# Kernel optimization log

Measured on AMD Instinct MI355X. Metric: run time of the kernel, lower is better.

Reference implementation:

```python
import jax, jax.numpy as jnp
import numpy as np

N_EMBD = 1024
N_HEAD = 16
B, T = 2, 2048

def setup_inputs() -> dict:
    key = jax.random.key(0)
    ks = jax.random.split(key, 5)
    s = 1.0 / np.sqrt(N_EMBD)
    return {
        'x': jax.random.normal(ks[0], (B, T, N_EMBD), jnp.float32),
        'W_attn': jax.random.normal(ks[1], (N_EMBD, 3 * N_EMBD), jnp.float32) * s,
        'b_attn': jax.random.normal(ks[2], (3 * N_EMBD,), jnp.float32) * 0.02,
        'W_proj': jax.random.normal(ks[3], (N_EMBD, N_EMBD), jnp.float32) * s,
        'b_proj': jax.random.normal(ks[4], (N_EMBD,), jnp.float32) * 0.02,
    }

def reference(x, W_attn, b_attn, W_proj, b_proj):
    Bx, Tx, C = x.shape
    H = N_HEAD
    D = C // H  # head dim
    qkv = x @ W_attn + b_attn                      # [B,T,3C]
    q, k, v = jnp.split(qkv, 3, axis=-1)
    # [B,T,C] -> [B,H,T,D]
    q = q.reshape(Bx, Tx, H, D).transpose(0, 2, 1, 3)
    k = k.reshape(Bx, Tx, H, D).transpose(0, 2, 1, 3)
    v = v.reshape(Bx, Tx, H, D).transpose(0, 2, 1, 3)
    scale = 1.0 / jnp.sqrt(jnp.asarray(D, x.dtype))
    scores = jnp.einsum('bhqd,bhkd->bhqk', q, k) * scale   # [B,H,T,T]
    causal = jnp.tril(jnp.ones((Tx, Tx), bool))
    scores = jnp.where(causal, scores, jnp.asarray(-jnp.inf, scores.dtype))
    attn = jax.nn.softmax(scores, axis=-1)
    y = jnp.einsum('bhqk,bhkd->bhqd', attn, v)              # [B,H,T,D]
    y = y.transpose(0, 2, 1, 3).reshape(Bx, Tx, C)
    return y @ W_proj + b_proj
```

## Files before the change

### kernel.cpp

```cpp
#include <hip/hip_runtime.h>
#include <stdint.h>

typedef float f32x4 __attribute__((ext_vector_type(4)));
typedef __bf16 bf16x8 __attribute__((ext_vector_type(8)));
typedef unsigned short ushort8 __attribute__((ext_vector_type(8)));
typedef unsigned short u16;

#define DEVINL static __device__ __forceinline__

#define EXP2(x) exp2f(x)

#define VMCNT(N)                                        \
  {                                                     \
    asm volatile("s_waitcnt vmcnt(" #N ")" ::: "memory"); \
    __builtin_amdgcn_sched_barrier(0);                  \
  }

DEVINL void barrier_raw() {
  __builtin_amdgcn_sched_barrier(0);
  __builtin_amdgcn_s_barrier();
  __builtin_amdgcn_sched_barrier(0);
}

DEVINL u16 f2bf(float f) {
  __bf16 h = (__bf16)f;
  return __builtin_bit_cast(u16, h);
}

DEVINL void gload16(const void* g, void* l) {
  __builtin_amdgcn_global_load_lds((__attribute__((address_space(1))) void*)g,
                                   (__attribute__((address_space(3))) void*)l, 16, 0, 0);
}

DEVINL f32x4 mfma16(bf16x8 a, bf16x8 b, f32x4 c) {
  return __builtin_amdgcn_mfma_f32_16x16x32_bf16(a, b, c, 0, 0, 0);
}

__global__ __launch_bounds__(256) void k_cast_bf16(const float* __restrict__ in,
                                                   u16* __restrict__ out) {
  const int i = blockIdx.x * 256 + threadIdx.x;
  const float4* p = (const float4*)in + (size_t)i * 2;
  float4 a = p[0], b = p[1];
  ushort8 o;
  o[0] = f2bf(a.x); o[1] = f2bf(a.y); o[2] = f2bf(a.z); o[3] = f2bf(a.w);
  o[4] = f2bf(b.x); o[5] = f2bf(b.y); o[6] = f2bf(b.z); o[7] = f2bf(b.w);
  *((ushort8*)out + i) = o;
}

__global__ __launch_bounds__(256) void k_tcast(const float* __restrict__ in,
                                               u16* __restrict__ out, int R, int C) {
  __shared__ float tile[32][33];
  const int tx = threadIdx.x & 31, ty = threadIdx.x >> 5;
  const int c0 = blockIdx.x * 32, r0 = blockIdx.y * 32;
#pragma unroll
  for (int k = 0; k < 4; ++k)
    tile[ty + k * 8][tx] = in[(size_t)(r0 + ty + k * 8) * C + (c0 + tx)];
  __syncthreads();
#pragma unroll
  for (int k = 0; k < 4; ++k)
    out[(size_t)(c0 + ty + k * 8) * R + (r0 + tx)] = f2bf(tile[tx][ty + k * 8]);
}

DEVINL void stage128x64(const u16* __restrict__ g, int ld, u16* lds, int t) {
#pragma unroll
  for (int i = 0; i < 4; ++i) {
    int ci = i * 256 + t;
    int row = ci >> 3, gr = ci & 7;
    int gs = gr ^ (row & 7);
    gload16(g + (size_t)row * ld + gs * 8, lds + ci * 8);
  }
}

DEVINL void gemm_core(const u16* __restrict__ A, const u16* __restrict__ B, int Kdim,
                      u16* As, u16* Bs, int t, f32x4 acc[4][4]) {
  const int l = t & 63, lr = l & 15, lg = l >> 4;
  const int wr = t >> 7, wc = (t >> 6) & 1;
  const int nk = Kdim >> 6;
  stage128x64(A, Kdim, As, t);
  stage128x64(B, Kdim, Bs, t);
  for (int kt = 0; kt < nk; ++kt) {
    if (kt + 1 < nk) {
      const int nx = ((kt + 1) & 1) * 8192;
      stage128x64(A + (kt + 1) * 64, Kdim, As + nx, t);
      stage128x64(B + (kt + 1) * 64, Kdim, Bs + nx, t);
      VMCNT(8);
    } else {
      VMCNT(0);
    }
    barrier_raw();
    const u16* Asc = As + (kt & 1) * 8192;
    const u16* Bsc = Bs + (kt & 1) * 8192;
#pragma unroll
    for (int ks = 0; ks < 2; ++ks) {
      bf16x8 af[4], bf[4];
#pragma unroll
      for (int mi = 0; mi < 4; ++mi) {
        int r = wr * 64 + mi * 16 + lr;
        int g = (ks * 4 + lg) ^ (r & 7);
        af[mi] = *(const bf16x8*)(Asc + r * 64 + g * 8);
      }
#pragma unroll
      for (int ni = 0; ni < 4; ++ni) {
        int r = wc * 64 + ni * 16 + lr;
        int g = (ks * 4 + lg) ^ (r & 7);
        bf[ni] = *(const bf16x8*)(Bsc + r * 64 + g * 8);
      }
#pragma unroll
      for (int mi = 0; mi < 4; ++mi)
#pragma unroll
        for (int ni = 0; ni < 4; ++ni)
          acc[mi][ni] = mfma16(af[mi], bf[ni], acc[mi][ni]);
    }
    barrier_raw();
  }
}

__global__ __launch_bounds__(256) void k_gemm_qkv(const u16* __restrict__ xb,
                                                  const u16* __restrict__ WaT,
                                                  const float* __restrict__ b_attn,
                                                  u16* __restrict__ Qo,
                                                  u16* __restrict__ Ko,
                                                  u16* __restrict__ Vto) {
  __shared__ u16 As[2 * 128 * 64], Bs[2 * 128 * 64];
  const int t = threadIdx.x;
  const int m0 = blockIdx.y * 128, n0 = blockIdx.x * 128;
  f32x4 acc[4][4] = {};
  gemm_core(xb + (size_t)m0 * 1024, WaT + (size_t)n0 * 1024, 1024, As, Bs, t, acc);
  const int l = t & 63, lr = l & 15, lg = l >> 4;
  const int wr = t >> 7, wc = (t >> 6) & 1;
#pragma unroll
  for (int ni = 0; ni < 4; ++ni) {
    const int gcol = n0 + wc * 64 + ni * 16 + lr;
    const int part = gcol >> 10;
    const int h = (gcol & 1023) >> 6, d = gcol & 63;
    const float bias = b_attn[gcol];
    if (part == 2) {
#pragma unroll
      for (int mi = 0; mi < 4; ++mi) {
        const int tt0 = m0 + wr * 64 + mi * 16 + lg * 4;
        const int bb = tt0 >> 11, tt = tt0 & 2047;
        ushort4 pk;
        pk.x = f2bf(acc[mi][ni][0] + bias);
        pk.y = f2bf(acc[mi][ni][1] + bias);
        pk.z = f2bf(acc[mi][ni][2] + bias);
        pk.w = f2bf(acc[mi][ni][3] + bias);
        *(ushort4*)(Vto + (size_t)(bb * 16 + h) * 131072 + (size_t)d * 2048 + tt) = pk;
      }
    } else {
      const float osc = (part == 0) ? 0.18033688f : 1.0f;
      u16* dst = (part == 0) ? Qo : Ko;
#pragma unroll
      for (int mi = 0; mi < 4; ++mi)
#pragma unroll
        for (int r = 0; r < 4; ++r) {
          const int grow = m0 + wr * 64 + mi * 16 + lg * 4 + r;
          const int bb = grow >> 11, tt = grow & 2047;
          dst[(size_t)((bb * 16 + h) * 2048 + tt) * 64 + d] =
              f2bf((acc[mi][ni][r] + bias) * osc);
        }
    }
  }
}

__global__ __launch_bounds__(256) void k_gemm_proj(const u16* __restrict__ Yb,
                                                   const u16* __restrict__ WpT,
                                                   const float* __restrict__ b_proj,
                                                   float* __restrict__ out) {
  __shared__ u16 As[2 * 128 * 64], Bs[2 * 128 * 64];
  const int t = threadIdx.x;
  const int m0 = blockIdx.y * 128, n0 = blockIdx.x * 128;
  f32x4 acc[4][4] = {};
  gemm_core(Yb + (size_t)m0 * 1024, WpT + (size_t)n0 * 1024, 1024, As, Bs, t, acc);
  const int l = t & 63, lr = l & 15, lg = l >> 4;
  const int wr = t >> 7, wc = (t >> 6) & 1;
#pragma unroll
  for (int ni = 0; ni < 4; ++ni) {
    const int gcol = n0 + wc * 64 + ni * 16 + lr;
    const float bias = b_proj[gcol];
#pragma unroll
    for (int mi = 0; mi < 4; ++mi)
#pragma unroll
      for (int r = 0; r < 4; ++r) {
        const int grow = m0 + wr * 64 + mi * 16 + lg * 4 + r;
        out[(size_t)grow * 1024 + gcol] = acc[mi][ni][r] + bias;
      }
  }
}

__global__ __launch_bounds__(512, 4) void k_flash(const u16* __restrict__ Q,
                                                  const u16* __restrict__ K,
                                                  const u16* __restrict__ Vt,
                                                  u16* __restrict__ Y) {
  __shared__ u16 Ks[2][64 * 64];
  __shared__ u16 Vs[2][64 * 64];
  __shared__ u16 Pl[8][16 * 40];
  __shared__ float Ms[4][64][18];
  const int t = threadIdx.x, l = t & 63, w = t >> 6, lr = l & 15, lg = l >> 4;
  const int wq = w & 3, wk = w >> 2;
  const int bid = blockIdx.x;
  const int j = bid >> 3;
  const int bh = (bid & 7) + 8 * (j >> 4);
  const int pr = j & 15;
  const size_t base = (size_t)bh * 131072;
  const int b = bh >> 4, hh = bh & 15;
  u16* Pw = Pl[w];
  const int prow = lr * 40;

  for (int half = 0; half < 2; ++half) {
    const int qt = half ? 31 - pr : pr;
    __syncthreads();
    {
      int row = t >> 3, g = t & 7, gs = g ^ (row & 7);
      gload16(K + base + (size_t)row * 64 + gs * 8, Ks[0] + t * 8);
      gload16(Vt + base + (size_t)row * 2048 + gs * 8, Vs[0] + t * 8);
    }
    const int qrow = qt * 64 + wq * 16 + lr;
    bf16x8 qf0 = *(const bf16x8*)(Q + base + (size_t)qrow * 64 + lg * 8);
    bf16x8 qf1 = *(const bf16x8*)(Q + base + (size_t)qrow * 64 + 32 + lg * 8);

    f32x4 accO[4] = {};
    float rs_lane = 0.f;

#define FLASH_STEP(CUR, KT)                                                          \
  {                                                                                  \
    if ((KT) < qt) {       \
      int row = t >> 3, g = t & 7, gs = g ^ (row & 7);                               \
      gload16(K + base + (size_t)(((KT) + 1) * 64 + row) * 64 + gs * 8,              \
              Ks[CUR ^ 1] + t * 8);                                                  \
      gload16(Vt + base + (size_t)row * 2048 + ((KT) + 1) * 64 + gs * 8,             \
              Vs[CUR ^ 1] + t * 8);                                                  \
      VMCNT(2);                                                                      \
    } else {                                                                         \
      VMCNT(0);                                                                      \
    }                                                                                \
    barrier_raw();                              \
    const bool full_skip = ((KT) == qt) && (wk == 1) && (wq < 2);                    \
    if (!full_skip) {                                                                \
      f32x4 st[2] = {};                                                              \
      __builtin_amdgcn_s_setprio(1);                                                 \
      _Pragma("unroll") for (int ni = 0; ni < 2; ++ni) {                             \
        const int r2 = wk * 32 + ni * 16 + lr, g0 = lg ^ (r2 & 7);                   \
        bf16x8 kb0 = *(const bf16x8*)(Ks[CUR] + r2 * 64 + g0 * 8);                   \
        bf16x8 kb1 = *(const bf16x8*)(Ks[CUR] + r2 * 64 + (g0 ^ 4) * 8);             \
        st[ni] = mfma16(kb0, qf0, st[ni]);                                           \
        st[ni] = mfma16(kb1, qf1, st[ni]);                                           \
      }                                                                              \
      __builtin_amdgcn_s_setprio(0);                                                 \
      if ((KT) == qt) {                                                              \
        const int ql = wq * 16 + lr;                                                 \
        _Pragma("unroll") for (int ni = 0; ni < 2; ++ni)                             \
          _Pragma("unroll") for (int r = 0; r < 4; ++r)                              \
            if (wk * 32 + ni * 16 + lg * 4 + r > ql) st[ni][r] = -1e30f;             \
      }                                                                              \
      _Pragma("unroll") for (int ni = 0; ni < 2; ++ni) {                             \
        float e0 = EXP2(st[ni][0]), e1 = EXP2(st[ni][1]);                            \
        float e2 = EXP2(st[ni][2]), e3 = EXP2(st[ni][3]);                            \
        rs_lane += (e0 + e1) + (e2 + e3);                                            \
        ushort4 pk;                                                                  \
        pk.x = f2bf(e0); pk.y = f2bf(e1); pk.z = f2bf(e2); pk.w = f2bf(e3);          \
        *(ushort4*)(Pw + prow + ni * 16 + lg * 4) = pk;                              \
      }                                                                              \
      bf16x8 pf = *(const bf16x8*)(Pw + prow + lg * 8);                              \
      __builtin_amdgcn_s_setprio(1);                                                 \
      _Pragma("unroll") for (int oi = 0; oi < 4; ++oi) {                             \
        const int rv = oi * 16 + lr;                                                 \
        bf16x8 vb =                                                                  \
            *(const bf16x8*)(Vs[CUR] + rv * 64 + (((wk * 4 + lg) ^ (rv & 7)) * 8));  \
        accO[oi] = mfma16(vb, pf, accO[oi]);                                         \
      }                                                                              \
      __builtin_amdgcn_s_setprio(0);                                                 \
    }                                                                                \
    barrier_raw();                          \
  }

    {
      int kt = 0;
      while (true) {
        FLASH_STEP(0, kt);
        if (++kt > qt) break;
        FLASH_STEP(1, kt);
        if (++kt > qt) break;
      }
    }
#undef FLASH_STEP

    float l_run = rs_lane;
    l_run += __shfl_xor(l_run, 16);
    l_run += __shfl_xor(l_run, 32);
    if (wk == 1) {
      float* Mp = &Ms[wq][l][0];
#pragma unroll
      for (int oi = 0; oi < 4; ++oi) *(f32x4*)(Mp + oi * 4) = accO[oi];
      Mp[16] = l_run;
    }
    __syncthreads();
    if (wk == 0) {
      const float* Mp = &Ms[wq][l][0];
      const float inv = 1.0f / (l_run + Mp[16]);
      const int yrow = b * 2048 + qrow;
#pragma unroll
      for (int oi = 0; oi < 4; ++oi) {
        f32x4 po = *(const f32x4*)(Mp + oi * 4);
        ushort4 o4;
        o4.x = f2bf((accO[oi][0] + po[0]) * inv);
        o4.y = f2bf((accO[oi][1] + po[1]) * inv);
        o4.z = f2bf((accO[oi][2] + po[2]) * inv);
        o4.w = f2bf((accO[oi][3] + po[3]) * inv);
        *(ushort4*)(Y + (size_t)yrow * 1024 + hh * 64 + oi * 16 + lg * 4) = o4;
      }
    }
  }
}

extern "C" void kernel_launch(void* const* d_in, const int* in_sizes, int n_in,
                              void* d_out, int out_size, void* d_ws, size_t ws_size,
                              hipStream_t stream) {
  const float* x      = (const float*)d_in[0];
  const float* W_attn = (const float*)d_in[1];
  const float* b_attn = (const float*)d_in[2];
  const float* W_proj = (const float*)d_in[3];
  const float* b_proj = (const float*)d_in[4];
  float* out = (float*)d_out;

  char* ws = (char*)d_ws;
  u16* xb  = (u16*)(ws);
  u16* WaT = (u16*)(ws + (8u  << 20));
  u16* WpT = (u16*)(ws + (14u << 20));
  u16* Qb  = (u16*)(ws + (16u << 20));
  u16* Kb  = (u16*)(ws + (24u << 20));
  u16* Vtb = (u16*)(ws + (32u << 20));
  u16* Yb  = (u16*)(ws + (40u << 20));

  k_cast_bf16<<<dim3(2048), dim3(256), 0, stream>>>(x, xb);
  k_tcast<<<dim3(96, 32), dim3(256), 0, stream>>>(W_attn, WaT, 1024, 3072);
  k_tcast<<<dim3(32, 32), dim3(256), 0, stream>>>(W_proj, WpT, 1024, 1024);
  k_gemm_qkv<<<dim3(24, 32), dim3(256), 0, stream>>>(xb, WaT, b_attn, Qb, Kb, Vtb);
  k_flash<<<dim3(512), dim3(512), 0, stream>>>(Qb, Kb, Vtb, Yb);
  k_gemm_proj<<<dim3(8, 32), dim3(256), 0, stream>>>(Yb, WpT, b_proj, out);
}
```

Baseline: 121.4 us.

## Rewrite flash attention with 32x32 MFMA, register-resident P, 128-row query tiles

The flash kernel switches from 16x16x32 to 32x32x16 bf16 MFMA, with each wave handling 32 query rows and 32 keys per tile. The probability tile now stays in registers, built with v_cvt_pk_bf16_f32 and v_permlane32_swap, so the LDS round trip for P is gone. Work is reorganised from paired causal halves of 64 rows to single 128-row query tiles with a reversed tile order. The aim is fewer MFMA and LDS instructions per tile, at the cost of more registers and a different load balance across blocks.

```diff
diff --git a/kernel.cpp b/kernel.cpp
--- a/kernel.cpp
+++ b/kernel.cpp
@@ -2,18 +2,20 @@
 #include <stdint.h>
 
 typedef float f32x4 __attribute__((ext_vector_type(4)));
+typedef float f32x16 __attribute__((ext_vector_type(16)));
 typedef __bf16 bf16x8 __attribute__((ext_vector_type(8)));
 typedef unsigned short ushort8 __attribute__((ext_vector_type(8)));
+typedef unsigned int uint4v __attribute__((ext_vector_type(4)));
 typedef unsigned short u16;
 
 #define DEVINL static __device__ __forceinline__
 
 #define EXP2(x) exp2f(x)
 
-#define VMCNT(N)                                        \
-  {                                                     \
+#define VMCNT(N)                                          \
+  {                                                       \
     asm volatile("s_waitcnt vmcnt(" #N ")" ::: "memory"); \
-    __builtin_amdgcn_sched_barrier(0);                  \
+    __builtin_amdgcn_sched_barrier(0);                    \
   }
 
 DEVINL void barrier_raw() {
@@ -27,6 +29,16 @@
   return __builtin_bit_cast(u16, h);
 }
 
+DEVINL unsigned cvtpk(float lo, float hi) {
+  unsigned r;
+  asm("v_cvt_pk_bf16_f32 %0, %1, %2" : "=v"(r) : "v"(lo), "v"(hi));
+  return r;
+}
+
+DEVINL void plswap(unsigned& a, unsigned& b) {
+  asm("v_permlane32_swap_b32 %0, %1" : "+v"(a), "+v"(b));
+}
+
 DEVINL void gload16(const void* g, void* l) {
   __builtin_amdgcn_global_load_lds((__attribute__((address_space(1))) void*)g,
                                    (__attribute__((address_space(3))) void*)l, 16, 0, 0);
@@ -34,6 +46,9 @@
 
 DEVINL f32x4 mfma16(bf16x8 a, bf16x8 b, f32x4 c) {
   return __builtin_amdgcn_mfma_f32_16x16x32_bf16(a, b, c, 0, 0, 0);
+}
+DEVINL f32x16 mfma32(bf16x8 a, bf16x8 b, f32x16 c) {
+  return __builtin_amdgcn_mfma_f32_32x32x16_bf16(a, b, c, 0, 0, 0);
 }
 
 __global__ __launch_bounds__(256) void k_cast_bf16(const float* __restrict__ in,
@@ -191,123 +206,141 @@
                                                   const u16* __restrict__ K,
                                                   const u16* __restrict__ Vt,
                                                   u16* __restrict__ Y) {
-  __shared__ u16 Ks[2][64 * 64];
-  __shared__ u16 Vs[2][64 * 64];
-  __shared__ u16 Pl[8][16 * 40];
-  __shared__ float Ms[4][64][18];
-  const int t = threadIdx.x, l = t & 63, w = t >> 6, lr = l & 15, lg = l >> 4;
+  __shared__ u16 Ks[2][4096];
+  __shared__ u16 Vs[2][4096];
+  __shared__ float Ms[4][64][33];
+  const int t = threadIdx.x, l = t & 63, w = t >> 6;
+  const int ql = l & 31, hi = l >> 5;
   const int wq = w & 3, wk = w >> 2;
   const int bid = blockIdx.x;
-  const int j = bid >> 3;
-  const int bh = (bid & 7) + 8 * (j >> 4);
-  const int pr = j & 15;
+  const int u = bid >> 3;
+  const int qt = 15 - (u >> 2);
+  const int bh = (bid & 7) + 8 * (u & 3);
   const size_t base = (size_t)bh * 131072;
   const int b = bh >> 4, hh = bh & 15;
-  u16* Pw = Pl[w];
-  const int prow = lr * 40;
-
-  for (int half = 0; half < 2; ++half) {
-    const int qt = half ? 31 - pr : pr;
-    __syncthreads();
-    {
-      int row = t >> 3, g = t & 7, gs = g ^ (row & 7);
-      gload16(K + base + (size_t)row * 64 + gs * 8, Ks[0] + t * 8);
-      gload16(Vt + base + (size_t)row * 2048 + gs * 8, Vs[0] + t * 8);
-    }
-    const int qrow = qt * 64 + wq * 16 + lr;
-    bf16x8 qf0 = *(const bf16x8*)(Q + base + (size_t)qrow * 64 + lg * 8);
-    bf16x8 qf1 = *(const bf16x8*)(Q + base + (size_t)qrow * 64 + 32 + lg * 8);
-
-    f32x4 accO[4] = {};
-    float rs_lane = 0.f;
-
-#define FLASH_STEP(CUR, KT)                                                          \
-  {                                                                                  \
-    if ((KT) < qt) {       \
-      int row = t >> 3, g = t & 7, gs = g ^ (row & 7);                               \
-      gload16(K + base + (size_t)(((KT) + 1) * 64 + row) * 64 + gs * 8,              \
-              Ks[CUR ^ 1] + t * 8);                                                  \
-      gload16(Vt + base + (size_t)row * 2048 + ((KT) + 1) * 64 + gs * 8,             \
-              Vs[CUR ^ 1] + t * 8);                                                  \
-      VMCNT(2);                                                                      \
-    } else {                                                                         \
-      VMCNT(0);                                                                      \
-    }                                                                                \
-    barrier_raw();                              \
-    const bool full_skip = ((KT) == qt) && (wk == 1) && (wq < 2);                    \
-    if (!full_skip) {                                                                \
-      f32x4 st[2] = {};                                                              \
-      __builtin_amdgcn_s_setprio(1);                                                 \
-      _Pragma("unroll") for (int ni = 0; ni < 2; ++ni) {                             \
-        const int r2 = wk * 32 + ni * 16 + lr, g0 = lg ^ (r2 & 7);                   \
-        bf16x8 kb0 = *(const bf16x8*)(Ks[CUR] + r2 * 64 + g0 * 8);                   \
-        bf16x8 kb1 = *(const bf16x8*)(Ks[CUR] + r2 * 64 + (g0 ^ 4) * 8);             \
-        st[ni] = mfma16(kb0, qf0, st[ni]);                                           \
-        st[ni] = mfma16(kb1, qf1, st[ni]);                                           \
-      }                                                                              \
-      __builtin_amdgcn_s_setprio(0);                                                 \
-      if ((KT) == qt) {                                                              \
-        const int ql = wq * 16 + lr;                                                 \
-        _Pragma("unroll") for (int ni = 0; ni < 2; ++ni)                             \
-          _Pragma("unroll") for (int r = 0; r < 4; ++r)                              \
-            if (wk * 32 + ni * 16 + lg * 4 + r > ql) st[ni][r] = -1e30f;             \
-      }                                                                              \
-      _Pragma("unroll") for (int ni = 0; ni < 2; ++ni) {                             \
-        float e0 = EXP2(st[ni][0]), e1 = EXP2(st[ni][1]);                            \
-        float e2 = EXP2(st[ni][2]), e3 = EXP2(st[ni][3]);                            \
-        rs_lane += (e0 + e1) + (e2 + e3);                                            \
-        ushort4 pk;                                                                  \
-        pk.x = f2bf(e0); pk.y = f2bf(e1); pk.z = f2bf(e2); pk.w = f2bf(e3);          \
-        *(ushort4*)(Pw + prow + ni * 16 + lg * 4) = pk;                              \
-      }                                                                              \
-      bf16x8 pf = *(const bf16x8*)(Pw + prow + lg * 8);                              \
-      __builtin_amdgcn_s_setprio(1);                                                 \
-      _Pragma("unroll") for (int oi = 0; oi < 4; ++oi) {                             \
-        const int rv = oi * 16 + lr;                                                 \
-        bf16x8 vb =                                                                  \
-            *(const bf16x8*)(Vs[CUR] + rv * 64 + (((wk * 4 + lg) ^ (rv & 7)) * 8));  \
-        accO[oi] = mfma16(vb, pf, accO[oi]);                                         \
-      }                                                                              \
-      __builtin_amdgcn_s_setprio(0);                                                 \
-    }                                                                                \
-    barrier_raw();                          \
-  }
-
-    {
-      int kt = 0;
-      while (true) {
-        FLASH_STEP(0, kt);
-        if (++kt > qt) break;
-        FLASH_STEP(1, kt);
-        if (++kt > qt) break;
-      }
-    }
-#undef FLASH_STEP
-
-    float l_run = rs_lane;
-    l_run += __shfl_xor(l_run, 16);
-    l_run += __shfl_xor(l_run, 32);
-    if (wk == 1) {
-      float* Mp = &Ms[wq][l][0];
-#pragma unroll
-      for (int oi = 0; oi < 4; ++oi) *(f32x4*)(Mp + oi * 4) = accO[oi];
-      Mp[16] = l_run;
-    }
-    __syncthreads();
-    if (wk == 0) {
-      const float* Mp = &Ms[wq][l][0];
-      const float inv = 1.0f / (l_run + Mp[16]);
-      const int yrow = b * 2048 + qrow;
-#pragma unroll
-      for (int oi = 0; oi < 4; ++oi) {
-        f32x4 po = *(const f32x4*)(Mp + oi * 4);
-        ushort4 o4;
-        o4.x = f2bf((accO[oi][0] + po[0]) * inv);
-        o4.y = f2bf((accO[oi][1] + po[1]) * inv);
-        o4.z = f2bf((accO[oi][2] + po[2]) * inv);
-        o4.w = f2bf((accO[oi][3] + po[3]) * inv);
-        *(ushort4*)(Y + (size_t)yrow * 1024 + hh * 64 + oi * 16 + lg * 4) = o4;
-      }
+  const int qbase = qt * 128 + wq * 32;
+  const int qrow = qbase + ql;
+  const int nkt = 2 * qt + 2;
+
+  bf16x8 qb[4];
+#pragma unroll
+  for (int m = 0; m < 4; ++m)
+    qb[m] = *(const bf16x8*)(Q + base + (size_t)qrow * 64 + hi * 8 + 16 * m);
+
+  {
+    int row = t >> 3, g = t & 7, gs = g ^ (row & 7);
+    gload16(K + base + (size_t)row * 64 + gs * 8, Ks[0] + t * 8);
+    gload16(Vt + base + (size_t)row * 2048 + gs * 8, Vs[0] + t * 8);
+  }
+
+  f32x16 accO0 = {}, accO1 = {};
+  float rs_lane = 0.f;
+  const int krow = wk * 32 + ql;
+  const int kswz = krow & 7;
+
+#define STEP(CUR, KT)                                                                 \
+  {                                                                                   \
+    if ((KT) + 1 < nkt) {                                                             \
+      int row = t >> 3, g = t & 7, gs = g ^ (row & 7);                                \
+      gload16(K + base + (size_t)(((KT) + 1) * 64 + row) * 64 + gs * 8,               \
+              Ks[CUR ^ 1] + t * 8);                                                   \
+      gload16(Vt + base + (size_t)row * 2048 + ((KT) + 1) * 64 + gs * 8,              \
+              Vs[CUR ^ 1] + t * 8);                                                   \
+      VMCNT(2);                                                                       \
+    } else {                                                                          \
+      VMCNT(0);                                                                       \
+    }                                                                                 \
+    barrier_raw();                               \
+    const int kbase = (KT) * 64 + wk * 32;                                            \
+    if (kbase <= qbase + 31) {                   \
+      f32x16 st = {};                                                                 \
+      __builtin_amdgcn_s_setprio(1);                                                  \
+      _Pragma("unroll") for (int m = 0; m < 4; ++m) {                                 \
+        bf16x8 ka = *(const bf16x8*)(Ks[CUR] + krow * 64 + (((hi + 2 * m) ^ kswz) * 8)); \
+        st = mfma32(ka, qb[m], st);                                                   \
+      }                                                                               \
+      __builtin_amdgcn_s_setprio(0);                                                  \
+      if (kbase + 31 > qbase) {                            \
+        _Pragma("unroll") for (int r = 0; r < 16; ++r) {                              \
+          const int keyl = (r & 3) + 8 * (r >> 2) + 4 * hi;                           \
+          if (kbase + keyl > qrow) st[r] = -1e30f;                                    \
+        }                                                                             \
+      }                                                                               \
+      float p[16];                                                                    \
+      _Pragma("unroll") for (int r = 0; r < 16; ++r) {                                \
+        p[r] = EXP2(st[r]);                                                           \
+        rs_lane += p[r];                                                              \
+      }                                                                               \
+      unsigned uu[8];                                                                 \
+      _Pragma("unroll") for (int i = 0; i < 8; ++i) uu[i] = cvtpk(p[2 * i], p[2 * i + 1]); \
+      plswap(uu[0], uu[2]);                                                           \
+      plswap(uu[1], uu[3]);                                                           \
+      plswap(uu[4], uu[6]);                                                           \
+      plswap(uu[5], uu[7]);                                                           \
+      uint4v w0 = {uu[0], uu[1], uu[2], uu[3]};                                       \
+      uint4v w1 = {uu[4], uu[5], uu[6], uu[7]};                                       \
+      bf16x8 pf0 = __builtin_bit_cast(bf16x8, w0);                                    \
+      bf16x8 pf1 = __builtin_bit_cast(bf16x8, w1);                                    \
+      __builtin_amdgcn_s_setprio(1);                                                  \
+      {                                                                               \
+        const int vr0 = ql, vz0 = vr0 & 7;                                            \
+        bf16x8 va0 = *(const bf16x8*)(Vs[CUR] + vr0 * 64 + (((wk * 4 + hi) ^ vz0) * 8)); \
+        bf16x8 va1 =                                                                  \
+            *(const bf16x8*)(Vs[CUR] + vr0 * 64 + (((wk * 4 + 2 + hi) ^ vz0) * 8));   \
+        accO0 = mfma32(va0, pf0, accO0);                                              \
+        accO0 = mfma32(va1, pf1, accO0);                                              \
+        const int vr1 = 32 + ql, vz1 = vr1 & 7;                                       \
+        bf16x8 vb0 = *(const bf16x8*)(Vs[CUR] + vr1 * 64 + (((wk * 4 + hi) ^ vz1) * 8)); \
+        bf16x8 vb1 =                                                                  \
+            *(const bf16x8*)(Vs[CUR] + vr1 * 64 + (((wk * 4 + 2 + hi) ^ vz1) * 8));   \
+        accO1 = mfma32(vb0, pf0, accO1);                                              \
+        accO1 = mfma32(vb1, pf1, accO1);                                              \
+      }                                                                               \
+      __builtin_amdgcn_s_setprio(0);                                                  \
+    }                                                                                 \
+    barrier_raw();                                   \
+  }
+
+  for (int kt = 0; kt < nkt; kt += 2) {
+    STEP(0, kt);
+    STEP(1, kt + 1);
+  }
+#undef STEP
+
+  rs_lane += __shfl_xor(rs_lane, 32);
+
+  if (wk == 1) {
+    float* Mp = &Ms[wq][l][0];
+#pragma unroll
+    for (int i = 0; i < 16; ++i) Mp[i] = accO0[i];
+#pragma unroll
+    for (int i = 0; i < 16; ++i) Mp[16 + i] = accO1[i];
+    Mp[32] = rs_lane;
+  }
+  __syncthreads();
+  if (wk == 0) {
+    const float* Mp = &Ms[wq][l][0];
+    const float inv = 1.0f / (rs_lane + Mp[32]);
+    u16* yb = Y + ((size_t)(b * 2048 + qrow)) * 1024 + hh * 64;
+#pragma unroll
+    for (int rq = 0; rq < 4; ++rq) {
+      const int d0 = 8 * rq + 4 * hi;
+      ushort4 o4;
+      o4.x = f2bf((accO0[rq * 4 + 0] + Mp[rq * 4 + 0]) * inv);
+      o4.y = f2bf((accO0[rq * 4 + 1] + Mp[rq * 4 + 1]) * inv);
+      o4.z = f2bf((accO0[rq * 4 + 2] + Mp[rq * 4 + 2]) * inv);
+      o4.w = f2bf((accO0[rq * 4 + 3] + Mp[rq * 4 + 3]) * inv);
+      *(ushort4*)(yb + d0) = o4;
+    }
+#pragma unroll
+    for (int rq = 0; rq < 4; ++rq) {
+      const int d0 = 32 + 8 * rq + 4 * hi;
+      ushort4 o4;
+      o4.x = f2bf((accO1[rq * 4 + 0] + Mp[16 + rq * 4 + 0]) * inv);
+      o4.y = f2bf((accO1[rq * 4 + 1] + Mp[16 + rq * 4 + 1]) * inv);
+      o4.z = f2bf((accO1[rq * 4 + 2] + Mp[16 + rq * 4 + 2]) * inv);
+      o4.w = f2bf((accO1[rq * 4 + 3] + Mp[16 + rq * 4 + 3]) * inv);
+      *(ushort4*)(yb + d0) = o4;
     }
   }
 }
```

New measurement: 121.9 us. Within noise of the previous version (+0.4%).
